# Kernel optimization log

Hardware: AMD Instinct MI355X
Metric: run time of the kernel (lower is better)

Reference implementation:

```python
import jax, jax.numpy as jnp
import numpy as np

N_NODES = 100000
N_EDGES = 1600000
D = 64
L = 3


def setup_inputs() -> dict:
    key = jax.random.key(0)
    ks = jax.random.split(key, 6)
    x = jax.random.normal(ks[0], (N_NODES, D), dtype=jnp.float32)
    edges = jax.random.randint(ks[1], (2, N_EDGES), 0, N_NODES, dtype=jnp.int64)
    scale = 1.0 / np.sqrt(D)
    W_phi = jax.random.normal(ks[2], (L, D, D), dtype=jnp.float32) * scale
    W_theta = jax.random.normal(ks[3], (L, D, D), dtype=jnp.float32) * scale
    W_out = jax.random.normal(ks[4], (1, D), dtype=jnp.float32) * scale
    b_out = jax.random.normal(ks[5], (1,), dtype=jnp.float32) * scale
    return {"x": x, "edges": edges, "W_phi": W_phi, "W_theta": W_theta,
            "W_out": W_out, "b_out": b_out}


def _devconv(x, Wp, Wt, src, dst):
    # DevConv: out_i = W_theta @ max_{j in N(i)} W_phi (x_j - x_i)
    diff = x[src] - x[dst]                 # [E, D] irregular gather
    msg = diff @ Wp.T                      # [E, D]
    agg = jax.ops.segment_max(msg, dst, num_segments=N_NODES)  # [N, D]
    agg = jnp.where(jnp.isneginf(agg), 0.0, agg)  # isolated nodes -> 0
    return agg @ Wt.T


def reference(x, edges, W_phi, W_theta, W_out, b_out):
    src, dst = edges[0], edges[1]
    for l in range(L):
        x = _devconv(x, W_phi[l], W_theta[l], src, dst)
    scores = (x @ W_out.T + b_out)[:, 0]   # Linear(D,1) then squeeze(-1)
    return jax.nn.sigmoid(scores)
```

## Files before the change

### kernel.cpp

```cpp
#include <hip/hip_runtime.h>
#include <math.h>


#define WBITS 9
#define WNODES 512
#define MAXNB 256
#define CHUNK 8192
#define STG_CAP 12288

#define PKNINF 0xFC00FC00u

typedef __fp16 h2v __attribute__((ext_vector_type(2)));
typedef _Float16 f16x8 __attribute__((ext_vector_type(8)));
typedef float f32x4 __attribute__((ext_vector_type(4)));

__device__ __forceinline__ unsigned pkmax(unsigned a, unsigned b) {
    unsigned r;
    asm("v_pk_max_f16 %0, %1, %2" : "=v"(r) : "v"(a), "v"(b));
    return r;
}
__device__ __forceinline__ unsigned pkrtz(float a, float b) {
    h2v r = __builtin_amdgcn_cvt_pkrtz(a, b);
    return *reinterpret_cast<unsigned*>(&r);
}
__device__ __forceinline__ float h2lo(unsigned u) {
    h2v h = *reinterpret_cast<h2v*>(&u);
    return (float)h.x;
}
__device__ __forceinline__ float h2hi(unsigned u) {
    h2v h = *reinterpret_cast<h2v*>(&u);
    return (float)h.y;
}

#define G8(K0) do { \
    int j0 = __builtin_amdgcn_ds_swizzle(myc, (((K0)+0)<<5)|0x10); \
    int j1 = __builtin_amdgcn_ds_swizzle(myc, (((K0)+1)<<5)|0x10); \
    int j2 = __builtin_amdgcn_ds_swizzle(myc, (((K0)+2)<<5)|0x10); \
    int j3 = __builtin_amdgcn_ds_swizzle(myc, (((K0)+3)<<5)|0x10); \
    int j4 = __builtin_amdgcn_ds_swizzle(myc, (((K0)+4)<<5)|0x10); \
    int j5 = __builtin_amdgcn_ds_swizzle(myc, (((K0)+5)<<5)|0x10); \
    int j6 = __builtin_amdgcn_ds_swizzle(myc, (((K0)+6)<<5)|0x10); \
    int j7 = __builtin_amdgcn_ds_swizzle(myc, (((K0)+7)<<5)|0x10); \
    uint2 w0 = y16[(size_t)j0 * 16 + t]; \
    uint2 w1 = y16[(size_t)j1 * 16 + t]; \
    uint2 w2 = y16[(size_t)j2 * 16 + t]; \
    uint2 w3 = y16[(size_t)j3 * 16 + t]; \
    uint2 w4 = y16[(size_t)j4 * 16 + t]; \
    uint2 w5 = y16[(size_t)j5 * 16 + t]; \
    uint2 w6 = y16[(size_t)j6 * 16 + t]; \
    uint2 w7 = y16[(size_t)j7 * 16 + t]; \
    c0 = pkmax(c0, pkmax(pkmax(pkmax(w0.x, w1.x), pkmax(w2.x, w3.x)), \
                         pkmax(pkmax(w4.x, w5.x), pkmax(w6.x, w7.x)))); \
    c1 = pkmax(c1, pkmax(pkmax(pkmax(w0.y, w1.y), pkmax(w2.y, w3.y)), \
                         pkmax(pkmax(w4.y, w5.y), pkmax(w6.y, w7.y)))); \
} while (0)

__global__ __launch_bounds__(256) void prep_k(
    const float* __restrict__ Wp, const float* __restrict__ Wt,
    const float* __restrict__ Wout,
    __fp16* __restrict__ Wh, float* __restrict__ vout,
    int* __restrict__ bcnt)
{
    __shared__ float A[4096];
    __shared__ float B[4096];
    int tid = threadIdx.x;
    int b = blockIdx.x;
    if (b < 2) {
        if (b == 0 && tid < MAXNB) bcnt[tid] = 0;
        const float* Ap = Wp + (size_t)(b + 1) * 4096;
        const float* Bp = Wt + (size_t)b * 4096;
        for (int i = tid; i < 4096; i += 256) { A[i] = Ap[i]; B[i] = Bp[i]; }
        __syncthreads();
        __fp16* C = Wh + (size_t)(b + 1) * 4096;
        for (int i = tid; i < 4096; i += 256) {
            int d = i >> 6, k = i & 63;
            float s = 0.f;
            #pragma unroll
            for (int m = 0; m < 64; ++m) s += A[d * 64 + m] * B[m * 64 + k];
            C[i] = (__fp16)s;
        }
    } else {
        for (int i = tid; i < 4096; i += 256) {
            A[i] = Wt[2 * 4096 + i];
            Wh[i] = (__fp16)Wp[i];
        }
        if (tid < 64) B[tid] = Wout[tid];
        __syncthreads();
        if (tid < 64) {
            float s = 0.f;
            #pragma unroll
            for (int m = 0; m < 64; ++m) s += B[m] * A[m * 64 + tid];
            vout[tid] = s;
        }
    }
}

__global__ __launch_bounds__(256) void hist_gemm_k(
    const int* __restrict__ eidx, int* __restrict__ bcnt, int E, int NB,
    int chunkBlocks,
    const float* __restrict__ xin, const __fp16* __restrict__ W,
    unsigned short* __restrict__ y16o, int n)
{
    __shared__ int h[MAXNB];
    int tid = threadIdx.x;
    if (blockIdx.x < chunkBlocks) {
        for (int i = tid; i < NB; i += 256) h[i] = 0;
        __syncthreads();
        int start = blockIdx.x * CHUNK;
        int end = min(E, start + CHUNK);
        for (int e = start + tid; e < end; e += 256)
            atomicAdd(&h[eidx[E + e] >> WBITS], 1);
        __syncthreads();
        for (int i = tid; i < NB; i += 256)
            if (h[i]) atomicAdd(&bcnt[i], h[i]);
    } else {
        int lane = tid & 63;
        int wid  = tid >> 6;
        int r0   = ((blockIdx.x - chunkBlocks) * 4 + wid) * 16;
        if (r0 >= n) return;
        int l15 = lane & 15;
        int ko  = (lane >> 4) * 8;

        f16x8 af[4][2];
        #pragma unroll
        for (int dt = 0; dt < 4; ++dt)
            #pragma unroll
            for (int kf = 0; kf < 2; ++kf)
                af[dt][kf] = *(const f16x8*)(W + (size_t)(dt * 16 + l15) * 64 + ko + kf * 32);

        f16x8 bf[2];
        int rr = min(r0 + l15, n - 1);
        #pragma unroll
        for (int kf = 0; kf < 2; ++kf) {
            const float4* p = (const float4*)(xin + (size_t)rr * 64 + ko + kf * 32);
            float4 a = p[0], b = p[1];
            union { uint4 u; f16x8 hh; } cv;
            cv.u.x = pkrtz(a.x, a.y); cv.u.y = pkrtz(a.z, a.w);
            cv.u.z = pkrtz(b.x, b.y); cv.u.w = pkrtz(b.z, b.w);
            bf[kf] = cv.hh;
        }

        int r = r0 + l15;
        int d4 = (lane >> 4) * 4;
        #pragma unroll
        for (int dt = 0; dt < 4; ++dt) {
            f32x4 acc = {0.f, 0.f, 0.f, 0.f};
            acc = __builtin_amdgcn_mfma_f32_16x16x32_f16(af[dt][0], bf[0], acc, 0, 0, 0);
            acc = __builtin_amdgcn_mfma_f32_16x16x32_f16(af[dt][1], bf[1], acc, 0, 0, 0);
            if (r < n) {
                uint2 p; p.x = pkrtz(acc[0], acc[1]); p.y = pkrtz(acc[2], acc[3]);
                *(uint2*)(y16o + (size_t)r * 64 + dt * 16 + d4) = p;
            }
        }
    }
}

__global__ __launch_bounds__(256) void bucket_scan_k(
    const int* __restrict__ bcnt, int* __restrict__ bbase,
    int* __restrict__ gcur, int* __restrict__ row_ptr, int NB, int N, int E)
{
    __shared__ int sA[MAXNB], sB[MAXNB];
    int tid = threadIdx.x;
    int v0 = (tid < NB) ? bcnt[tid] : 0;
    sA[tid] = v0;
    __syncthreads();
    int* sp = sA; int* dp = sB;
    for (int off = 1; off < MAXNB; off <<= 1) {
        dp[tid] = sp[tid] + ((tid >= off) ? sp[tid - off] : 0);
        __syncthreads();
        int* t = sp; sp = dp; dp = t;
    }
    if (tid < NB) {
        int ex = sp[tid] - v0;
        bbase[tid] = ex;
        gcur[tid]  = ex;
    }
    if (tid == 0) {
        bbase[NB]  = E;
        row_ptr[N] = E;
    }
}

__global__ __launch_bounds__(256) void partA_k(
    const int* __restrict__ eidx, int* __restrict__ gcur,
    int* __restrict__ B1, int E, int NB)
{
    __shared__ int hist[MAXNB];
    __shared__ int lofs[MAXNB];
    __shared__ int lcur[MAXNB];
    __shared__ int gofs[MAXNB];
    __shared__ int sA[MAXNB], sB[MAXNB];
    __shared__ int stg_val[CHUNK];
    __shared__ int stg_pos[CHUNK];
    int tid = threadIdx.x;
    int start = blockIdx.x * CHUNK;
    int cnt = min(E - start, CHUNK);
    if (cnt <= 0) return;

    for (int i = tid; i < NB; i += 256) hist[i] = 0;
    __syncthreads();

    int es[CHUNK / 256], ed[CHUNK / 256];
    #pragma unroll
    for (int i = 0; i < CHUNK / 256; ++i) {
        int li = i * 256 + tid;
        if (li < cnt) {
            es[i] = eidx[start + li];
            ed[i] = eidx[E + start + li];
            atomicAdd(&hist[ed[i] >> WBITS], 1);
        }
    }
    __syncthreads();
    sA[tid] = (tid < NB) ? hist[tid] : 0;
    __syncthreads();
    int* sp = sA; int* dp = sB;
    for (int off = 1; off < MAXNB; off <<= 1) {
        dp[tid] = sp[tid] + ((tid >= off) ? sp[tid - off] : 0);
        __syncthreads();
        int* t = sp; sp = dp; dp = t;
    }
    if (tid < NB) {
        int c  = hist[tid];
        int ex = sp[tid] - c;
        lofs[tid] = ex;
        lcur[tid] = ex;
        gofs[tid] = c ? atomicAdd(&gcur[tid], c) : 0;
    }
    __syncthreads();
    #pragma unroll
    for (int i = 0; i < CHUNK / 256; ++i) {
        int li = i * 256 + tid;
        if (li < cnt) {
            int b = ed[i] >> WBITS;
            int p = atomicAdd(&lcur[b], 1);
            stg_val[p] = es[i] | ((ed[i] & (WNODES - 1)) << 17);
            stg_pos[p] = gofs[b] + (p - lofs[b]);
        }
    }
    __syncthreads();
    for (int i = tid; i < cnt; i += 256)
        B1[stg_pos[i]] = stg_val[i];
}

__global__ __launch_bounds__(256) void partB_k(
    const int* __restrict__ B1, const int* __restrict__ bbase,
    int* __restrict__ row_ptr, int* __restrict__ col, int N, int NB)
{
    __shared__ int cnt[WNODES];
    __shared__ int lcur[WNODES];
    __shared__ int sA[WNODES], sB[WNODES];
    __shared__ int stg[STG_CAP];
    int b   = blockIdx.x;
    int tid = threadIdx.x;
    int gb0 = bbase[b], gb1 = bbase[b + 1];
    int m   = gb1 - gb0;
    int nb0 = b << WBITS;

    for (int i = tid; i < WNODES; i += 256) cnt[i] = 0;
    __syncthreads();
    for (int i = tid; i < m; i += 256)
        atomicAdd(&cnt[B1[gb0 + i] >> 17], 1);
    __syncthreads();
    for (int i = tid; i < WNODES; i += 256) sA[i] = cnt[i];
    __syncthreads();
    int* sp = sA; int* dp = sB;
    for (int off = 1; off < WNODES; off <<= 1) {
        for (int i = tid; i < WNODES; i += 256)
            dp[i] = sp[i] + ((i >= off) ? sp[i - off] : 0);
        __syncthreads();
        int* t = sp; sp = dp; dp = t;
    }
    for (int i = tid; i < WNODES; i += 256) {
        int ex = sp[i] - cnt[i];
        lcur[i] = ex;
        int node = nb0 + i;
        if (node < N) row_ptr[node] = gb0 + ex;
    }
    __syncthreads();
    if (m <= STG_CAP) {
        for (int i = tid; i < m; i += 256) {
            int v = B1[gb0 + i];
            int p = atomicAdd(&lcur[v >> 17], 1);
            stg[p] = v & 0x1FFFF;
        }
        __syncthreads();
        for (int i = tid; i < m; i += 256)
            col[gb0 + i] = stg[i];
    } else {
        for (int i = tid; i < m; i += 256) {
            int v = B1[gb0 + i];
            int p = atomicAdd(&lcur[v >> 17], 1);
            col[gb0 + p] = v & 0x1FFFF;
        }
    }
}

template<bool HEAD>
__global__ __launch_bounds__(256) void gather_fused_k(
    const int* __restrict__ rp, const int* __restrict__ col,
    const uint2* __restrict__ y16,
    const __fp16* __restrict__ W,
    unsigned short* __restrict__ y16o,
    const float* __restrict__ vv, const float* __restrict__ bptr,
    float* __restrict__ out, int n)
{
    __shared__ __fp16 sAgg[4][16][80];
    int lane = threadIdx.x & 63;
    int wid  = threadIdx.x >> 6;
    int q = lane >> 4, t = lane & 15;
    int base = blockIdx.x * 64 + wid * 16;

    for (int p = 0; p < 4; ++p) {
        int node  = base + p * 4 + q;
        bool alive = node < n;
        int beg = 0, cnt = 0;
        if (alive) { beg = rp[node]; cnt = rp[node + 1] - beg; }
        unsigned c0 = PKNINF, c1 = PKNINF;
        if (cnt > 0) {
            int pcnt = (cnt + 7) & ~7;
            int e = 0;
            while (e < pcnt) {
                int myc = col[beg + min(e + t, cnt - 1)];
                G8(0);
                if (e + 8 < pcnt) { G8(8); }
                e += 16;
            }
        }
        if (alive) {
            bool has = cnt > 0;
            uint2 yi2 = y16[(size_t)node * 16 + t];
            float g0 = has ? (h2lo(c0) - h2lo(yi2.x)) : 0.f;
            float g1 = has ? (h2hi(c0) - h2hi(yi2.x)) : 0.f;
            float g2 = has ? (h2lo(c1) - h2lo(yi2.y)) : 0.f;
            float g3 = has ? (h2hi(c1) - h2hi(yi2.y)) : 0.f;
            if (!HEAD) {
                uint2 pk; pk.x = pkrtz(g0, g1); pk.y = pkrtz(g2, g3);
                *(uint2*)&sAgg[wid][p * 4 + q][4 * t] = pk;
            } else {
                float4 vp = ((const float4*)vv)[t];
                float s = g0 * vp.x + g1 * vp.y + g2 * vp.z + g3 * vp.w;
                s += __shfl_xor(s, 8);
                s += __shfl_xor(s, 4);
                s += __shfl_xor(s, 2);
                s += __shfl_xor(s, 1);
                if (t == 0)
                    out[node] = 1.f / (1.f + __expf(-(s + bptr[0])));
            }
        } else if (!HEAD) {
            uint2 z; z.x = 0u; z.y = 0u;
            *(uint2*)&sAgg[wid][p * 4 + q][4 * t] = z;
        }
    }

    if (!HEAD) {
        __syncthreads();
        f16x8 af[4][2];
        #pragma unroll
        for (int dt = 0; dt < 4; ++dt)
            #pragma unroll
            for (int kf = 0; kf < 2; ++kf)
                af[dt][kf] = *(const f16x8*)(W + (size_t)(dt * 16 + t) * 64 + q * 8 + kf * 32);
        f16x8 bf[2];
        #pragma unroll
        for (int kf = 0; kf < 2; ++kf)
            bf[kf] = *(const f16x8*)&sAgg[wid][t][q * 8 + kf * 32];

        int r = base + t;
        int d4 = q * 4;
        #pragma unroll
        for (int dt = 0; dt < 4; ++dt) {
            f32x4 acc = {0.f, 0.f, 0.f, 0.f};
            acc = __builtin_amdgcn_mfma_f32_16x16x32_f16(af[dt][0], bf[0], acc, 0, 0, 0);
            acc = __builtin_amdgcn_mfma_f32_16x16x32_f16(af[dt][1], bf[1], acc, 0, 0, 0);
            if (r < n) {
                uint2 pk; pk.x = pkrtz(acc[0], acc[1]); pk.y = pkrtz(acc[2], acc[3]);
                *(uint2*)(y16o + (size_t)r * 64 + dt * 16 + d4) = pk;
            }
        }
    }
}

extern "C" void kernel_launch(void* const* d_in, const int* in_sizes, int n_in,
                              void* d_out, int out_size, void* d_ws, size_t ws_size,
                              hipStream_t stream)
{
    const float* x     = (const float*)d_in[0];
    const int*   edges = (const int*)d_in[1];
    const float* Wp    = (const float*)d_in[2];
    const float* Wt    = (const float*)d_in[3];
    const float* Wout  = (const float*)d_in[4];
    const float* bout  = (const float*)d_in[5];
    const int N = in_sizes[0] / 64;
    const int E = in_sizes[1] / 2;
    const int NB = (N + WNODES - 1) >> WBITS;
    float* out = (float*)d_out;

    char* ws = (char*)d_ws;
    unsigned short* y16A = (unsigned short*)ws; ws += (size_t)N * 64 * 2;
    unsigned short* y16B = (unsigned short*)ws; ws += (size_t)N * 64 * 2;
    int*   B1  = (int*)y16B;
    int* col     = (int*)ws; ws += (size_t)(E + 8) * 4;
    int* row_ptr = (int*)ws; ws += (size_t)(N + 4) * 4;
    int* bcnt    = (int*)ws; ws += MAXNB * 4;
    int* bbase   = (int*)ws; ws += (MAXNB + 4) * 4;
    int* gcur    = (int*)ws; ws += MAXNB * 4;
    __fp16* Wh = (__fp16*)ws; ws += 3 * 4096 * 2;
    float*  vv = (float*)ws;  ws += 64 * 4;

    const int chunkBlocks = (E + CHUNK - 1) / CHUNK;
    const int gemmBlocks  = ((N + 15) / 16 + 3) / 4;
    const int fusedBlocks = (N + 63) / 64;

    prep_k<<<3, 256, 0, stream>>>(Wp, Wt, Wout, Wh, vv, bcnt);

    hist_gemm_k<<<chunkBlocks + gemmBlocks, 256, 0, stream>>>(
        edges, bcnt, E, NB, chunkBlocks, x, Wh, y16A, N);
    bucket_scan_k<<<1, 256, 0, stream>>>(bcnt, bbase, gcur, row_ptr, NB, N, E);
    partA_k<<<chunkBlocks, 256, 0, stream>>>(edges, gcur, B1, E, NB);
    partB_k<<<NB, 256, 0, stream>>>(B1, bbase, row_ptr, col, N, NB);

    gather_fused_k<false><<<fusedBlocks, 256, 0, stream>>>(
        row_ptr, col, (const uint2*)y16A, Wh + 4096, y16B,
        nullptr, nullptr, nullptr, N);
    gather_fused_k<false><<<fusedBlocks, 256, 0, stream>>>(
        row_ptr, col, (const uint2*)y16B, Wh + 8192, y16A,
        nullptr, nullptr, nullptr, N);
    gather_fused_k<true><<<fusedBlocks, 256, 0, stream>>>(
        row_ptr, col, (const uint2*)y16A, nullptr, nullptr,
        vv, bout, out, N);
}
```

Before: 181.2 us.

## Fold bucket scan into partition kernels and use finer buckets

Result: no change. 183.8 us (+1.4%).

```diff
diff --git a/kernel.cpp b/kernel.cpp
--- a/kernel.cpp
+++ b/kernel.cpp
@@ -2,10 +2,10 @@
 #include <math.h>
 
 
-#define WBITS 9
-#define WNODES 512
-#define MAXNB 256
-#define CHUNK 8192
+#define WBITS 8
+#define WNODES 256
+#define MAXNB 512
+#define CHUNK 4096
 #define STG_CAP 12288
 
 #define PKNINF 0xFC00FC00u
@@ -59,14 +59,19 @@
     const float* __restrict__ Wp, const float* __restrict__ Wt,
     const float* __restrict__ Wout,
     __fp16* __restrict__ Wh, float* __restrict__ vout,
-    int* __restrict__ bcnt)
+    int* __restrict__ bcnt, int* __restrict__ gcur,
+    int* __restrict__ row_ptr, int N, int E)
 {
     __shared__ float A[4096];
     __shared__ float B[4096];
     int tid = threadIdx.x;
     int b = blockIdx.x;
     if (b < 2) {
-        if (b == 0 && tid < MAXNB) bcnt[tid] = 0;
+        if (b == 0) {
+            for (int i = tid; i < MAXNB; i += 256) { bcnt[i] = 0; gcur[i] = 0; }
+        } else if (tid == 0) {
+            row_ptr[N] = E;
+        }
         const float* Ap = Wp + (size_t)(b + 1) * 4096;
         const float* Bp = Wt + (size_t)b * 4096;
         for (int i = tid; i < 4096; i += 256) { A[i] = Ap[i]; B[i] = Bp[i]; }
@@ -104,7 +109,7 @@
     __shared__ int h[MAXNB];
     int tid = threadIdx.x;
     if (blockIdx.x < chunkBlocks) {
-        for (int i = tid; i < NB; i += 256) h[i] = 0;
+        for (int i = tid; i < MAXNB; i += 256) h[i] = 0;
         __syncthreads();
         int start = blockIdx.x * CHUNK;
         int end = min(E, start + CHUNK);
@@ -155,35 +160,9 @@
     }
 }
 
-__global__ __launch_bounds__(256) void bucket_scan_k(
-    const int* __restrict__ bcnt, int* __restrict__ bbase,
-    int* __restrict__ gcur, int* __restrict__ row_ptr, int NB, int N, int E)
-{
-    __shared__ int sA[MAXNB], sB[MAXNB];
-    int tid = threadIdx.x;
-    int v0 = (tid < NB) ? bcnt[tid] : 0;
-    sA[tid] = v0;
-    __syncthreads();
-    int* sp = sA; int* dp = sB;
-    for (int off = 1; off < MAXNB; off <<= 1) {
-        dp[tid] = sp[tid] + ((tid >= off) ? sp[tid - off] : 0);
-        __syncthreads();
-        int* t = sp; sp = dp; dp = t;
-    }
-    if (tid < NB) {
-        int ex = sp[tid] - v0;
-        bbase[tid] = ex;
-        gcur[tid]  = ex;
-    }
-    if (tid == 0) {
-        bbase[NB]  = E;
-        row_ptr[N] = E;
-    }
-}
-
 __global__ __launch_bounds__(256) void partA_k(
-    const int* __restrict__ eidx, int* __restrict__ gcur,
-    int* __restrict__ B1, int E, int NB)
+    const int* __restrict__ eidx, const int* __restrict__ bcnt,
+    int* __restrict__ gcur, int* __restrict__ B1, int E, int NB)
 {
     __shared__ int hist[MAXNB];
     __shared__ int lofs[MAXNB];
@@ -197,7 +176,7 @@
     int cnt = min(E - start, CHUNK);
     if (cnt <= 0) return;
 
-    for (int i = tid; i < NB; i += 256) hist[i] = 0;
+    for (int i = tid; i < MAXNB; i += 256) hist[i] = 0;
     __syncthreads();
 
     int es[CHUNK / 256], ed[CHUNK / 256];
@@ -211,20 +190,32 @@
         }
     }
     __syncthreads();
-    sA[tid] = (tid < NB) ? hist[tid] : 0;
+    for (int i = tid; i < MAXNB; i += 256) sA[i] = (i < NB) ? bcnt[i] : 0;
     __syncthreads();
     int* sp = sA; int* dp = sB;
     for (int off = 1; off < MAXNB; off <<= 1) {
-        dp[tid] = sp[tid] + ((tid >= off) ? sp[tid - off] : 0);
+        for (int i = tid; i < MAXNB; i += 256)
+            dp[i] = sp[i] + ((i >= off) ? sp[i - off] : 0);
         __syncthreads();
         int* t = sp; sp = dp; dp = t;
     }
-    if (tid < NB) {
-        int c  = hist[tid];
-        int ex = sp[tid] - c;
-        lofs[tid] = ex;
-        lcur[tid] = ex;
-        gofs[tid] = c ? atomicAdd(&gcur[tid], c) : 0;
+    for (int i = tid; i < MAXNB; i += 256)
+        gofs[i] = sp[i] - ((i < NB) ? bcnt[i] : 0);
+    __syncthreads();
+    for (int i = tid; i < MAXNB; i += 256) sp[i] = hist[i];
+    __syncthreads();
+    for (int off = 1; off < MAXNB; off <<= 1) {
+        for (int i = tid; i < MAXNB; i += 256)
+            dp[i] = sp[i] + ((i >= off) ? sp[i - off] : 0);
+        __syncthreads();
+        int* t = sp; sp = dp; dp = t;
+    }
+    for (int i = tid; i < MAXNB; i += 256) {
+        int c  = hist[i];
+        int ex = sp[i] - c;
+        lofs[i] = ex;
+        lcur[i] = ex;
+        if (c) gofs[i] += atomicAdd(&gcur[i], c);
     }
     __syncthreads();
     #pragma unroll
@@ -243,37 +234,48 @@
 }
 
 __global__ __launch_bounds__(256) void partB_k(
-    const int* __restrict__ B1, const int* __restrict__ bbase,
+    const int* __restrict__ B1, const int* __restrict__ bcnt,
     int* __restrict__ row_ptr, int* __restrict__ col, int N, int NB)
 {
     __shared__ int cnt[WNODES];
     __shared__ int lcur[WNODES];
-    __shared__ int sA[WNODES], sB[WNODES];
+    __shared__ int sA[MAXNB], sB[MAXNB];
     __shared__ int stg[STG_CAP];
     int b   = blockIdx.x;
     int tid = threadIdx.x;
-    int gb0 = bbase[b], gb1 = bbase[b + 1];
+
+    for (int i = tid; i < MAXNB; i += 256) sA[i] = (i < NB) ? bcnt[i] : 0;
+    __syncthreads();
+    int* sp = sA; int* dp = sB;
+    for (int off = 1; off < MAXNB; off <<= 1) {
+        for (int i = tid; i < MAXNB; i += 256)
+            dp[i] = sp[i] + ((i >= off) ? sp[i - off] : 0);
+        __syncthreads();
+        int* t = sp; sp = dp; dp = t;
+    }
+    int gb1 = sp[b];
+    int gb0 = gb1 - bcnt[b];
     int m   = gb1 - gb0;
     int nb0 = b << WBITS;
 
-    for (int i = tid; i < WNODES; i += 256) cnt[i] = 0;
+    if (tid < WNODES) cnt[tid] = 0;
     __syncthreads();
     for (int i = tid; i < m; i += 256)
         atomicAdd(&cnt[B1[gb0 + i] >> 17], 1);
     __syncthreads();
-    for (int i = tid; i < WNODES; i += 256) sA[i] = cnt[i];
-    __syncthreads();
-    int* sp = sA; int* dp = sB;
+    int v0 = (tid < WNODES) ? cnt[tid] : 0;
+    sA[tid] = v0;
+    __syncthreads();
+    sp = sA; dp = sB;
     for (int off = 1; off < WNODES; off <<= 1) {
-        for (int i = tid; i < WNODES; i += 256)
-            dp[i] = sp[i] + ((i >= off) ? sp[i - off] : 0);
+        dp[tid] = sp[tid] + ((tid >= off) ? sp[tid - off] : 0);
         __syncthreads();
         int* t = sp; sp = dp; dp = t;
     }
-    for (int i = tid; i < WNODES; i += 256) {
-        int ex = sp[i] - cnt[i];
-        lcur[i] = ex;
-        int node = nb0 + i;
+    if (tid < WNODES) {
+        int ex = sp[tid] - v0;
+        lcur[tid] = ex;
+        int node = nb0 + tid;
         if (node < N) row_ptr[node] = gb0 + ex;
     }
     __syncthreads();
@@ -402,7 +404,6 @@
     int* col     = (int*)ws; ws += (size_t)(E + 8) * 4;
     int* row_ptr = (int*)ws; ws += (size_t)(N + 4) * 4;
     int* bcnt    = (int*)ws; ws += MAXNB * 4;
-    int* bbase   = (int*)ws; ws += (MAXNB + 4) * 4;
     int* gcur    = (int*)ws; ws += MAXNB * 4;
     __fp16* Wh = (__fp16*)ws; ws += 3 * 4096 * 2;
     float*  vv = (float*)ws;  ws += 64 * 4;
@@ -411,13 +412,12 @@
     const int gemmBlocks  = ((N + 15) / 16 + 3) / 4;
     const int fusedBlocks = (N + 63) / 64;
 
-    prep_k<<<3, 256, 0, stream>>>(Wp, Wt, Wout, Wh, vv, bcnt);
+    prep_k<<<3, 256, 0, stream>>>(Wp, Wt, Wout, Wh, vv, bcnt, gcur, row_ptr, N, E);
 
     hist_gemm_k<<<chunkBlocks + gemmBlocks, 256, 0, stream>>>(
         edges, bcnt, E, NB, chunkBlocks, x, Wh, y16A, N);
-    bucket_scan_k<<<1, 256, 0, stream>>>(bcnt, bbase, gcur, row_ptr, NB, N, E);
-    partA_k<<<chunkBlocks, 256, 0, stream>>>(edges, gcur, B1, E, NB);
-    partB_k<<<NB, 256, 0, stream>>>(B1, bbase, row_ptr, col, N, NB);
+    partA_k<<<chunkBlocks, 256, 0, stream>>>(edges, bcnt, gcur, B1, E, NB);
+    partB_k<<<NB, 256, 0, stream>>>(B1, bcnt, row_ptr, col, N, NB);
 
     gather_fused_k<false><<<fusedBlocks, 256, 0, stream>>>(
         row_ptr, col, (const uint2*)y16A, Wh + 4096, y16B,
```
